# Optimization experiments

Measured on AMD Instinct MI355X. Metric: run time of the kernel, lower is better.

## Reference

```python
import jax, jax.numpy as jnp
import numpy as np

N = 50000
E = 1600000
IN_DIM = 64
EMB_DIM = 64
DENSE = 128
HEADS = 2
GATD = 64
SLOPE = 0.2


def gat_conv(x, src, dst, W, al, ar, b):
    # DGL GATConv: x [N, Fin], W [Fin, H*D], al/ar/b [H, D]
    n = x.shape[0]
    H, D = al.shape
    z = (x @ W).reshape(n, H, D)                      # [N,H,D]
    el = jnp.sum(z * al, axis=-1)                     # [N,H]
    er = jnp.sum(z * ar, axis=-1)                     # [N,H]
    e = jax.nn.leaky_relu(el[src] + er[dst], SLOPE)   # [E,H]
    # edge softmax grouped by destination node
    m = jax.ops.segment_max(e, dst, num_segments=n)   # [N,H]
    ex = jnp.exp(e - m[dst])                          # [E,H]
    s = jax.ops.segment_sum(ex, dst, num_segments=n)  # [N,H]
    alpha = ex / s[dst]                               # [E,H]
    out = jax.ops.segment_sum(alpha[:, :, None] * z[src], dst, num_segments=n)
    return out + b                                    # [N,H,D]


def setup_inputs() -> dict:
    key = jax.random.key(0)
    ks = jax.random.split(key, 20)
    g = lambda k, sh: jax.random.normal(k, sh, dtype=jnp.float32) * 0.05
    inp = {
        "feat": jax.random.normal(ks[0], (N, IN_DIM), dtype=jnp.float32),
        "node_ids": jax.random.randint(ks[1], (N,), 0, N, dtype=jnp.int32),
        "src": jax.random.randint(ks[2], (E,), 0, N, dtype=jnp.int32),
        "dst": jax.random.randint(ks[3], (E,), 0, N, dtype=jnp.int32),
        "emb": g(ks[4], (N, EMB_DIM)),
        "dense_w": g(ks[5], (IN_DIM + EMB_DIM, DENSE)),
        "dense_b": jnp.zeros((DENSE,), jnp.float32),
        "g1_w": g(ks[6], (DENSE, HEADS * GATD)),
        "g1_al": g(ks[7], (HEADS, GATD)),
        "g1_ar": g(ks[8], (HEADS, GATD)),
        "g1_b": jnp.zeros((HEADS, GATD), jnp.float32),
        "g2_w": g(ks[9], (HEADS * GATD, HEADS * GATD)),
        "g2_al": g(ks[10], (HEADS, GATD)),
        "g2_ar": g(ks[11], (HEADS, GATD)),
        "g2_b": jnp.zeros((HEADS, GATD), jnp.float32),
        "out_w": g(ks[12], (HEADS * GATD, 1)),
        "out_al": g(ks[13], (1, 1)),
        "out_ar": g(ks[14], (1, 1)),
        "out_b": jnp.zeros((1, 1), jnp.float32),
    }
    return inp


def reference(feat, node_ids, src, dst, emb, dense_w, dense_b,
              g1_w, g1_al, g1_ar, g1_b, g2_w, g2_al, g2_ar, g2_b,
              out_w, out_al, out_ar, out_b):
    # embedding concat + initial dense + ReLU
    h = jnp.concatenate([emb[node_ids], feat], axis=-1)   # [N, 128]
    h = jax.nn.relu(h @ dense_w + dense_b)                # [N, 128]
    # GAT layer 1: ReLU then concat heads (reshape N, H*D)
    h = jax.nn.relu(gat_conv(h, src, dst, g1_w, g1_al, g1_ar, g1_b))
    h = h.reshape(h.shape[0], -1)                         # [N, H*D]
    # GAT layer 2
    h = jax.nn.relu(gat_conv(h, src, dst, g2_w, g2_al, g2_ar, g2_b))
    h = h.reshape(h.shape[0], -1)
    # output GAT layer, 1 head, squeeze head dim
    h = gat_conv(h, src, dst, out_w, out_al, out_ar, out_b)  # [N,1,1]
    return h[:, 0, :]                                        # [N,1]
```

## Files before the change

kernel.cpp:

```cpp
#include <hip/hip_runtime.h>
#include <cfloat>
#include <cmath>


#define CBG 256
#define CAPC 12288
#define TILE 4096
#define BIMG 10240

typedef __attribute__((ext_vector_type(8))) short short8v;
typedef __attribute__((ext_vector_type(4))) float f32x4;

__device__ __forceinline__ float lrelu(float x) { return x > 0.f ? x : 0.2f * x; }

__device__ __forceinline__ uint32_t bf16_rne(float f) {
  uint32_t u = __float_as_uint(f);
  return (u + 0x7fffu + ((u >> 16) & 1u)) >> 16;
}
__device__ __forceinline__ uint32_t pack_hilo(float v) {
  uint32_t h = bf16_rne(v);
  float r = v - __uint_as_float(h << 16);
  return (h << 16) | bf16_rne(r);
}

__global__ __launch_bounds__(256) void prep_kernel(
    const float* __restrict__ W0, const float* __restrict__ W1,
    const float* __restrict__ W2, short* __restrict__ Whi0,
    short* __restrict__ Wlo0, short* __restrict__ Whi1, short* __restrict__ Wlo1,
    short* __restrict__ Whi2, short* __restrict__ Wlo2,
    int* __restrict__ scount, int ncb) {
  if (blockIdx.x >= 24) {
    for (int i = threadIdx.x; i < ncb; i += 256) scount[i] = 0;
    return;
  }
  int which = blockIdx.x >> 3;
  const float* W = which == 0 ? W0 : (which == 1 ? W1 : W2);
  short* Whi = which == 0 ? Whi0 : (which == 1 ? Whi1 : Whi2);
  short* Wlo = which == 0 ? Wlo0 : (which == 1 ? Wlo1 : Wlo2);
  int fid = (blockIdx.x & 7) * 256 + threadIdx.x;
  int lane = fid & 63;
  int cq = fid >> 6;
  int q = cq >> 3, c = cq & 7;
  int col = c * 16 + (lane & 15);
  int k0 = q * 32 + (lane >> 4) * 8;
#pragma unroll
  for (int j = 0; j < 8; j++) {
    float v = W[(k0 + j) * 128 + col];
    uint32_t h = bf16_rne(v);
    float r = v - __uint_as_float(h << 16);
    Whi[fid * 8 + j] = (short)h;
    Wlo[fid * 8 + j] = (short)bf16_rne(r);
  }
}

__global__ __launch_bounds__(256) void bucketA_kernel(
    const int* __restrict__ src, const int* __restrict__ dst,
    int* __restrict__ scount, uint32_t* __restrict__ tmp, int e, int ncb) {
  __shared__ int cnt[256];
  __shared__ int lscan[256];
  __shared__ int gbase[256];
  __shared__ uint32_t image[TILE];
  const int t = threadIdx.x;
  const int e0 = blockIdx.x * TILE;
  const int ne = min(TILE, e - e0);

  for (int i = t; i < 256; i += 256) cnt[i] = 0;
  __syncthreads();
  for (int i = t; i < ne; i += 256) atomicAdd(&cnt[dst[e0 + i] >> 8], 1);
  __syncthreads();
  if (t < 64) {
    int carry = 0;
    for (int base = 0; base < ncb; base += 64) {
      int idx = base + t;
      int c = (idx < ncb) ? cnt[idx] : 0;
      int v = c;
#pragma unroll
      for (int off = 1; off < 64; off <<= 1) {
        int u = __shfl_up(v, off, 64);
        if (t >= off) v += u;
      }
      if (idx < ncb) lscan[idx] = carry + v - c;
      carry += __shfl(v, 63, 64);
    }
  }
  __syncthreads();
  for (int b = t; b < ncb; b += 256)
    gbase[b] = (cnt[b] > 0) ? atomicAdd(&scount[b], cnt[b]) : 0;
  __syncthreads();
  for (int b = t; b < ncb; b += 256) cnt[b] = 0;
  __syncthreads();
  for (int i = t; i < ne; i += 256) {
    int d = dst[e0 + i], s = src[e0 + i];
    int b = d >> 8;
    int r = atomicAdd(&cnt[b], 1);
    image[lscan[b] + r] =
        (uint32_t)s | ((uint32_t)(d & 255) << 16) | ((uint32_t)b << 24);
  }
  __syncthreads();
  for (int j = t; j < ne; j += 256) {
    uint32_t w = image[j];
    int b = w >> 24;
    int pos = gbase[b] + (j - lscan[b]);
    if (pos < CAPC) tmp[(size_t)b * CAPC + pos] = w & 0xFFFFFFu;
  }
}

__device__ __forceinline__ void bucketB_body(
    int b, char* smem, const uint32_t* __restrict__ tmp,
    const int* __restrict__ scount, int* __restrict__ row_start,
    int* __restrict__ csr_src, int n, int ncb, int e, int sshift) {
  int* cnt2 = (int*)smem;
  int* wsum = cnt2 + 2048;
  int* s_base = wsum + 4;
  uint32_t* image = (uint32_t*)(smem + 8224);
  const int t = threadIdx.x, lane = t & 63, wid = t >> 6;

  if (t < 64) {
    int part = 0;
    for (int idx = lane; idx < b; idx += 64) part += scount[idx];
#pragma unroll
    for (int off = 32; off; off >>= 1) part += __shfl_xor(part, off, 64);
    if (lane == 0) *s_base = part;
  }
#pragma unroll
  for (int j = 0; j < 8; j++) cnt2[t * 8 + j] = 0;
  __syncthreads();
  const int total = min(scount[b], CAPC);
  const int base = *s_base;
  const uint32_t* strm = tmp + (size_t)b * CAPC;

  for (int i = t; i < total; i += 256) {
    uint32_t w = strm[i];
    int key = (((w >> 16) & 255) << 3) + ((w & 0xFFFFu) >> sshift);
    atomicAdd(&cnt2[key], 1);
  }
  __syncthreads();
  int c8[8];
  int run = 0;
#pragma unroll
  for (int j = 0; j < 8; j++) { int x = cnt2[t * 8 + j]; c8[j] = run; run += x; }
  int c = run, v = c;
#pragma unroll
  for (int off = 1; off < 64; off <<= 1) {
    int u = __shfl_up(v, off, 64);
    if (lane >= off) v += u;
  }
  if (lane == 63) wsum[wid] = v;
  __syncthreads();
  if (t == 0) {
    int acc = 0;
#pragma unroll
    for (int w = 0; w < 4; w++) { int x = wsum[w]; wsum[w] = acc; acc += x; }
  }
  __syncthreads();
  int ex = wsum[wid] + v - c;
#pragma unroll
  for (int j = 0; j < 8; j++) cnt2[t * 8 + j] = ex + c8[j];
  int d = b * CBG + t;
  if (d < n) row_start[d] = base + ex;
  if (b == 0 && t == 0) row_start[n] = e;
  __syncthreads();
  for (int i = t; i < total; i += 256) {
    uint32_t w = strm[i];
    uint32_t s = w & 0xFFFFu;
    int key = (((w >> 16) & 255) << 3) + (s >> sshift);
    int pos = atomicAdd(&cnt2[key], 1);
    if (pos < BIMG) image[pos] = s;
    else csr_src[base + pos] = (int)s;
  }
  __syncthreads();
  const int lim = total < BIMG ? total : BIMG;
  for (int j = t; j < lim; j += 256) csr_src[base + j] = (int)image[j];
}

template <int MODE>
__device__ __forceinline__ void mfmm_body(
    int bid, char* smem,
    const uint32_t* __restrict__ Xp, const short* __restrict__ Whi,
    const short* __restrict__ Wlo, const float* __restrict__ bias,
    uint32_t* __restrict__ Hp, uint32_t* __restrict__ zp,
    float2* __restrict__ el2, float2* __restrict__ er2,
    const float* __restrict__ al, const float* __restrict__ ar, int n,
    const float* __restrict__ emb, const int* __restrict__ ids,
    const float* __restrict__ feat) {
  short* Ahi = (short*)smem;
  short* Alo = Ahi + 64 * 136;
  const int t = threadIdx.x;
  const int nb = bid * 64;

  for (int idx = t; idx < 64 * 32; idx += 256) {
    int nl = idx >> 5, k4 = (idx & 31) << 2;
    int node = nb + nl;
    uint32_t h01 = 0, h23 = 0, l01 = 0, l23 = 0;
    if (node < n) {
      if (MODE == 1) {
        uint4 w = *(const uint4*)&Xp[(size_t)node * 128 + k4];
        h01 = (w.x >> 16) | (w.y & 0xffff0000u);
        l01 = (w.x & 0xffffu) | (w.y << 16);
        h23 = (w.z >> 16) | (w.w & 0xffff0000u);
        l23 = (w.z & 0xffffu) | (w.w << 16);
      } else {
        float4 v;
        if (k4 < 64) v = *(const float4*)&emb[(size_t)ids[node] * 64 + k4];
        else         v = *(const float4*)&feat[(size_t)node * 64 + (k4 - 64)];
        uint32_t a0 = bf16_rne(v.x), a1 = bf16_rne(v.y);
        uint32_t a2 = bf16_rne(v.z), a3 = bf16_rne(v.w);
        h01 = a0 | (a1 << 16);
        h23 = a2 | (a3 << 16);
        l01 = bf16_rne(v.x - __uint_as_float(a0 << 16)) |
              (bf16_rne(v.y - __uint_as_float(a1 << 16)) << 16);
        l23 = bf16_rne(v.z - __uint_as_float(a2 << 16)) |
              (bf16_rne(v.w - __uint_as_float(a3 << 16)) << 16);
      }
    }
    *(uint2*)&Ahi[nl * 136 + k4] = make_uint2(h01, h23);
    *(uint2*)&Alo[nl * 136 + k4] = make_uint2(l01, l23);
  }
  __syncthreads();

  const int lane = t & 63, wv = t >> 6;
  const int r16 = lane & 15, g = lane >> 4;
  const int arow = (wv * 16 + r16) * 136;

  f32x4 acc[8];
#pragma unroll
  for (int c = 0; c < 8; c++) acc[c] = (f32x4){0.f, 0.f, 0.f, 0.f};

#pragma unroll
  for (int q = 0; q < 4; q++) {
    int ka = q * 32 + g * 8;
    short8v ahi = *(const short8v*)&Ahi[arow + ka];
    short8v alo = *(const short8v*)&Alo[arow + ka];
#pragma unroll
    for (int c = 0; c < 8; c++) {
      short8v bhi = *(const short8v*)&Whi[(((q * 8 + c) * 64) + lane) * 8];
      short8v blo = *(const short8v*)&Wlo[(((q * 8 + c) * 64) + lane) * 8];
      acc[c] = __builtin_amdgcn_mfma_f32_16x16x32_bf16(ahi, bhi, acc[c], 0, 0, 0);
      acc[c] = __builtin_amdgcn_mfma_f32_16x16x32_bf16(ahi, blo, acc[c], 0, 0, 0);
      acc[c] = __builtin_amdgcn_mfma_f32_16x16x32_bf16(alo, bhi, acc[c], 0, 0, 0);
    }
  }

  const int node_base = nb + wv * 16;
  if (MODE == 0) {
#pragma unroll
    for (int c = 0; c < 8; c++) {
      int col = c * 16 + r16;
      float bv = bias[col];
#pragma unroll
      for (int r = 0; r < 4; r++) {
        int node = node_base + g * 4 + r;
        if (node < n) {
          float v = fmaxf(acc[c][r] + bv, 0.f);
          Hp[(size_t)node * 128 + col] = pack_hilo(v);
        }
      }
    }
  } else {
    float p0l[4] = {0, 0, 0, 0}, p1l[4] = {0, 0, 0, 0};
    float p0r[4] = {0, 0, 0, 0}, p1r[4] = {0, 0, 0, 0};
#pragma unroll
    for (int c = 0; c < 8; c++) {
      int col = c * 16 + r16;
      float av = al[col], rv = ar[col];
#pragma unroll
      for (int r = 0; r < 4; r++) {
        if (c < 4) { p0l[r] = fmaf(acc[c][r], av, p0l[r]); p0r[r] = fmaf(acc[c][r], rv, p0r[r]); }
        else       { p1l[r] = fmaf(acc[c][r], av, p1l[r]); p1r[r] = fmaf(acc[c][r], rv, p1r[r]); }
      }
    }
#pragma unroll
    for (int c = 0; c < 8; c++) {
#pragma unroll
      for (int r = 0; r < 4; r++) {
        float other = __shfl_xor(acc[c][r], 1, 64);
        int node = node_base + g * 4 + r;
        if (!(lane & 1) && node < n) {
          uint32_t w = bf16_rne(acc[c][r]) | (bf16_rne(other) << 16);
          zp[(size_t)node * 64 + c * 8 + (r16 >> 1)] = w;
        }
      }
    }
#pragma unroll
    for (int off = 1; off < 16; off <<= 1) {
#pragma unroll
      for (int r = 0; r < 4; r++) {
        p0l[r] += __shfl_xor(p0l[r], off, 64);
        p1l[r] += __shfl_xor(p1l[r], off, 64);
        p0r[r] += __shfl_xor(p0r[r], off, 64);
        p1r[r] += __shfl_xor(p1r[r], off, 64);
      }
    }
    if (r16 == 0) {
#pragma unroll
      for (int r = 0; r < 4; r++) {
        int node = node_base + g * 4 + r;
        if (node < n) {
          el2[node] = make_float2(p0l[r], p1l[r]);
          er2[node] = make_float2(p0r[r], p1r[r]);
        }
      }
    }
  }
}

__global__ __launch_bounds__(256) void mfmm0_bktB_kernel(
    const uint32_t* __restrict__ tmp, const int* __restrict__ scount,
    int* __restrict__ row_start, int* __restrict__ csr_src, int ncbB,
    const short* __restrict__ Whi, const short* __restrict__ Wlo,
    const float* __restrict__ bias, uint32_t* __restrict__ Hp, int n, int ncb,
    int e, int sshift, const float* __restrict__ emb, const int* __restrict__ ids,
    const float* __restrict__ feat) {
  __shared__ __align__(16) char smem[49200];
  if ((int)blockIdx.x < ncbB) {
    bucketB_body(blockIdx.x, smem, tmp, scount, row_start, csr_src, n, ncb, e,
                 sshift);
  } else {
    mfmm_body<0>(blockIdx.x - ncbB, smem, nullptr, Whi, Wlo, bias, Hp,
                 nullptr, nullptr, nullptr, nullptr, nullptr, n, emb, ids, feat);
  }
}

__global__ __launch_bounds__(256) void mfmm1_kernel(
    const uint32_t* __restrict__ Xp, const short* __restrict__ Whi,
    const short* __restrict__ Wlo, uint32_t* __restrict__ zp,
    float2* __restrict__ el2, float2* __restrict__ er2,
    const float* __restrict__ al, const float* __restrict__ ar, int n) {
  __shared__ __align__(16) char smem[34816];
  mfmm_body<1>(blockIdx.x, smem, Xp, Whi, Wlo, nullptr, nullptr, zp, el2, er2,
               al, ar, n, nullptr, nullptr, nullptr);
}

__global__ void hist_kernel(const int* __restrict__ dst, int* __restrict__ cnt, int e) {
  for (int i = blockIdx.x * blockDim.x + threadIdx.x; i < e; i += gridDim.x * blockDim.x)
    atomicAdd(&cnt[dst[i]], 1);
}
__global__ void scatter_kernel(const int* __restrict__ src, const int* __restrict__ dst,
                               const int* __restrict__ row_start, int* __restrict__ cursor,
                               int* __restrict__ csr_src, int e) {
  for (int i = blockIdx.x * blockDim.x + threadIdx.x; i < e; i += gridDim.x * blockDim.x) {
    int d = dst[i];
    int pos = atomicAdd(&cursor[d], 1);
    csr_src[row_start[d] + pos] = src[i];
  }
}
__global__ __launch_bounds__(1024) void scan1_kernel(const int* __restrict__ cnt,
                                                     int* __restrict__ row_start,
                                                     int* __restrict__ bsum, int n) {
  __shared__ int wsum[16];
  const int t = threadIdx.x, lane = t & 63, wid = t >> 6;
  int i = blockIdx.x * 1024 + t;
  int c = (i < n) ? cnt[i] : 0;
  int v = c;
#pragma unroll
  for (int off = 1; off < 64; off <<= 1) {
    int u = __shfl_up(v, off, 64);
    if (lane >= off) v += u;
  }
  if (lane == 63) wsum[wid] = v;
  __syncthreads();
  if (t == 0) {
    int acc = 0;
#pragma unroll
    for (int w = 0; w < 16; w++) { int x = wsum[w]; wsum[w] = acc; acc += x; }
    bsum[blockIdx.x] = acc;
  }
  __syncthreads();
  if (i < n) row_start[i] = wsum[wid] + v - c;
}
__global__ __launch_bounds__(64) void scan2_kernel(int* __restrict__ bsum, int nb) {
  const int lane = threadIdx.x;
  int carry = 0;
  for (int base = 0; base < nb; base += 64) {
    int idx = base + lane;
    int c = (idx < nb) ? bsum[idx] : 0;
    int v = c;
#pragma unroll
    for (int off = 1; off < 64; off <<= 1) {
      int u = __shfl_up(v, off, 64);
      if (lane >= off) v += u;
    }
    if (idx < nb) bsum[idx] = carry + v - c;
    carry += __shfl(v, 63, 64);
  }
}
__global__ void scan3_kernel(int* __restrict__ row_start, const int* __restrict__ bsum,
                             int n, int e) {
  int i = blockIdx.x * blockDim.x + threadIdx.x;
  if (i < n) row_start[i] += bsum[i >> 10];
  if (i == 0) row_start[n] = e;
}

#define CAP 256
__global__ __launch_bounds__(256) void agg12_kernel(
    const uint32_t* __restrict__ zp, const float2* __restrict__ el2,
    const float2* __restrict__ er2, const int* __restrict__ row_start,
    const int* __restrict__ csr_src, const float* __restrict__ bias,
    uint32_t* __restrict__ Hp,
    const float* __restrict__ ow, const float* __restrict__ oal,
    const float* __restrict__ oar, float* __restrict__ z3,
    float* __restrict__ el3, float* __restrict__ er3, int n, int fuse_out) {
  __shared__ float ecf[4][2][CAP];
  __shared__ int sc[4][CAP];
  const int w = threadIdx.x >> 6, lane = threadIdx.x & 63;
  const int node = blockIdx.x * 4 + w;
  const bool valid = node < n;
  int rs = 0, deg = 0;
  float er0 = 0.f, er1 = 0.f;
  if (valid) {
    rs = row_start[node];
    deg = row_start[node + 1] - rs;
    float2 e2 = er2[node];
    er0 = e2.x; er1 = e2.y;
  }
  const int cdeg = deg < CAP ? deg : CAP;

  float sp0 = 0.f, sp1 = 0.f;
  for (int i = lane; i < deg; i += 64) {
    int s = csr_src[rs + i];
    float2 l = el2[s];
    float x0 = __expf(lrelu(l.x + er0));
    float x1 = __expf(lrelu(l.y + er1));
    if (i < CAP) { sc[w][i] = s << 8; ecf[w][0][i] = x0; ecf[w][1][i] = x1; }
    sp0 += x0; sp1 += x1;
  }
#pragma unroll
  for (int off = 32; off; off >>= 1) {
    sp0 += __shfl_xor(sp0, off, 64);
    sp1 += __shfl_xor(sp1, off, 64);
  }
  __syncthreads();

  const float* exh = ecf[w][lane >> 5];
  const char* zpB = (const char*)zp + (size_t)lane * 4;
  float ae = 0.f, ao = 0.f;
  int i = 0;
  for (; i + 8 <= cdeg; i += 8) {
    uint32_t zw[8];
    float xh[8];
#pragma unroll
    for (int u = 0; u < 8; u++) {
      int off = sc[w][i + u];
      xh[u] = exh[i + u];
      zw[u] = *(const uint32_t*)(zpB + off);
    }
#pragma unroll
    for (int u = 0; u < 8; u++) {
      ae = fmaf(xh[u], __uint_as_float(zw[u] << 16), ae);
      ao = fmaf(xh[u], __uint_as_float(zw[u] & 0xffff0000u), ao);
    }
  }
  for (; i < cdeg; i++) {
    int off = sc[w][i];
    float x = exh[i];
    uint32_t zw = *(const uint32_t*)(zpB + off);
    ae = fmaf(x, __uint_as_float(zw << 16), ae);
    ao = fmaf(x, __uint_as_float(zw & 0xffff0000u), ao);
  }
  for (; i < deg; i++) {
    int s = csr_src[rs + i];
    float2 l = el2[s];
    float x0 = __expf(lrelu(l.x + er0));
    float x1 = __expf(lrelu(l.y + er1));
    float x = (lane < 32) ? x0 : x1;
    uint32_t zw = *(const uint32_t*)(zpB + ((size_t)s << 8));
    ae = fmaf(x, __uint_as_float(zw << 16), ae);
    ao = fmaf(x, __uint_as_float(zw & 0xffff0000u), ao);
  }

  if (valid) {
    float sp = (lane < 32) ? sp0 : sp1;
    float2 b2 = reinterpret_cast<const float2*>(bias)[lane];
    float oe, oo;
    if (deg == 0) { oe = b2.x; oo = b2.y; }
    else { oe = ae / sp + b2.x; oo = ao / sp + b2.y; }
    oe = fmaxf(oe, 0.f);
    oo = fmaxf(oo, 0.f);
    if (!fuse_out) {
      *(uint2*)&Hp[(size_t)node * 128 + 2 * lane] =
          make_uint2(pack_hilo(oe), pack_hilo(oo));
    } else {
      float2 w2 = reinterpret_cast<const float2*>(ow)[lane];
      float d = oe * w2.x + oo * w2.y;
#pragma unroll
      for (int off = 32; off; off >>= 1) d += __shfl_xor(d, off, 64);
      if (lane == 0) {
        z3[node] = d;
        el3[node] = d * oal[0];
        er3[node] = d * oar[0];
      }
    }
  }
}

__global__ __launch_bounds__(256) void agg3_kernel(
    const float* __restrict__ z3, const float* __restrict__ el3,
    const float* __restrict__ er3, const int* __restrict__ row_start,
    const int* __restrict__ csr_src, const float* __restrict__ b,
    float* __restrict__ out, int n) {
  int node = blockIdx.x * 8 + (threadIdx.x >> 5);
  int l32 = threadIdx.x & 31;
  if (node >= n) return;
  int rs = row_start[node];
  int deg = row_start[node + 1] - rs;
  float er = er3[node];
  float sp = 0.f, ap = 0.f;
  for (int i = l32; i < deg; i += 32) {
    int s = csr_src[rs + i];
    float ex = __expf(lrelu(el3[s] + er));
    sp += ex;
    ap = fmaf(ex, z3[s], ap);
  }
#pragma unroll
  for (int off = 16; off; off >>= 1) {
    sp += __shfl_xor(sp, off, 64);
    ap += __shfl_xor(ap, off, 64);
  }
  if (l32 == 0) out[node] = (deg == 0) ? b[0] : (ap / sp + b[0]);
}

extern "C" void kernel_launch(void* const* d_in, const int* in_sizes, int n_in,
                              void* d_out, int out_size, void* d_ws, size_t ws_size,
                              hipStream_t stream) {
  const float* feat     = (const float*)d_in[0];
  const int*   node_ids = (const int*)d_in[1];
  const int*   src      = (const int*)d_in[2];
  const int*   dst      = (const int*)d_in[3];
  const float* emb      = (const float*)d_in[4];
  const float* dense_w  = (const float*)d_in[5];
  const float* dense_b  = (const float*)d_in[6];
  const float* g1_w     = (const float*)d_in[7];
  const float* g1_al    = (const float*)d_in[8];
  const float* g1_ar    = (const float*)d_in[9];
  const float* g1_b     = (const float*)d_in[10];
  const float* g2_w     = (const float*)d_in[11];
  const float* g2_al    = (const float*)d_in[12];
  const float* g2_ar    = (const float*)d_in[13];
  const float* g2_b     = (const float*)d_in[14];
  const float* out_w    = (const float*)d_in[15];
  const float* out_al   = (const float*)d_in[16];
  const float* out_ar   = (const float*)d_in[17];
  const float* out_b    = (const float*)d_in[18];
  const int n = in_sizes[0] / 64;
  const int e = in_sizes[2];

  const int ncb = (n + CBG - 1) / CBG;
  int lg = 0;
  while ((1 << lg) < n) lg++;
  const int sshift = lg > 3 ? lg - 3 : 0;

  char* ws = (char*)d_ws;
  size_t off = 0;
  auto alloc = [&](size_t bytes) -> void* {
    void* p = ws + off;
    off += (bytes + 255) & ~(size_t)255;
    return p;
  };
  uint32_t* Hp       = (uint32_t*)alloc((size_t)n * 128 * 4);
  size_t zp_bytes    = (size_t)n * 64 * 4;
  size_t tmp_bytes   = (size_t)ncb * CAPC * 4;
  uint32_t* zp       = (uint32_t*)alloc(zp_bytes > tmp_bytes ? zp_bytes : tmp_bytes);
  uint32_t* tmp      = zp;
  float2*   el2      = (float2*)alloc((size_t)n * 8);
  float2*   er2      = (float2*)alloc((size_t)n * 8);
  float*    z3       = (float*)alloc((size_t)n * 4);
  float*    el3      = (float*)alloc((size_t)n * 4);
  float*    er3      = (float*)alloc((size_t)n * 4);
  int*      scount   = (int*)alloc((size_t)ncb * 4);
  int*      row_start= (int*)alloc((size_t)(n + 1) * 4);
  int*      csr_src  = (int*)alloc((size_t)e * 4);
  short*    Wd_hi    = (short*)alloc(2048 * 8 * 2);
  short*    Wd_lo    = (short*)alloc(2048 * 8 * 2);
  short*    W1_hi    = (short*)alloc(2048 * 8 * 2);
  short*    W1_lo    = (short*)alloc(2048 * 8 * 2);
  short*    W2_hi    = (short*)alloc(2048 * 8 * 2);
  short*    W2_lo    = (short*)alloc(2048 * 8 * 2);
  int*      cnt      = (int*)alloc((size_t)n * 4);
  int*      cursor   = (int*)alloc((size_t)n * 4);
  const int nblk     = (n + 1023) / 1024;
  int*      bsum     = (int*)alloc((size_t)nblk * 4);

  const int mmgrid = (n + 63) / 64;
  const int ngrid4 = (n + 3) / 4;
  const int ngrid8 = (n + 7) / 8;

  prep_kernel<<<25, 256, 0, stream>>>(dense_w, g1_w, g2_w,
                                      Wd_hi, Wd_lo, W1_hi, W1_lo, W2_hi, W2_lo,
                                      scount, ncb);

  if (n < 65536) {
    const int natile = (e + TILE - 1) / TILE;
    bucketA_kernel<<<natile, 256, 0, stream>>>(src, dst, scount, tmp, e, ncb);
    mfmm0_bktB_kernel<<<ncb + mmgrid, 256, 0, stream>>>(
        tmp, scount, row_start, csr_src, ncb,
        Wd_hi, Wd_lo, dense_b, Hp, n, ncb, e, sshift, emb, node_ids, feat);
  } else {
    hipMemsetAsync(cnt, 0, (size_t)n * 4, stream);
    hipMemsetAsync(cursor, 0, (size_t)n * 4, stream);
    hist_kernel<<<2048, 256, 0, stream>>>(dst, cnt, e);
    scan1_kernel<<<nblk, 1024, 0, stream>>>(cnt, row_start, bsum, n);
    scan2_kernel<<<1, 64, 0, stream>>>(bsum, nblk);
    scan3_kernel<<<(n + 255) / 256, 256, 0, stream>>>(row_start, bsum, n, e);
    scatter_kernel<<<2048, 256, 0, stream>>>(src, dst, row_start, cursor, csr_src, e);
    mfmm0_bktB_kernel<<<mmgrid, 256, 0, stream>>>(
        tmp, scount, row_start, csr_src, 0,
        Wd_hi, Wd_lo, dense_b, Hp, n, ncb, e, sshift, emb, node_ids, feat);
  }

  mfmm1_kernel<<<mmgrid, 256, 0, stream>>>(Hp, W1_hi, W1_lo, zp, el2, er2,
                                           g1_al, g1_ar, n);
  agg12_kernel<<<ngrid4, 256, 0, stream>>>(zp, el2, er2, row_start, csr_src, g1_b, Hp,
                                           nullptr, nullptr, nullptr, nullptr, nullptr,
                                           nullptr, n, 0);
  mfmm1_kernel<<<mmgrid, 256, 0, stream>>>(Hp, W2_hi, W2_lo, zp, el2, er2,
                                           g2_al, g2_ar, n);
  agg12_kernel<<<ngrid4, 256, 0, stream>>>(zp, el2, er2, row_start, csr_src, g2_b, nullptr,
                                           out_w, out_al, out_ar, z3, el3, er3, n, 1);
  agg3_kernel<<<ngrid8, 256, 0, stream>>>(z3, el3, er3, row_start, csr_src, out_b,
                                          (float*)d_out, n);
}
```

Before: 232.7 us.

## Use half-wave per node in GAT aggregation with 8-byte gathers

The agg12 kernel now gives each destination node a 32-lane half-wavefront instead of a full 64-lane wavefront, so a block handles 8 nodes. Each lane gathers an 8-byte chunk (four bf16 features) per source row instead of 4 bytes, and the output store and bias load widen to match. This halves the lanes spent per node, which should help since the mean degree is about 32, and it issues fewer, wider gather loads. In exchange each lane carries more accumulators and the unroll drops to 4, and LDS use per block doubles, which may cut occupancy.

Result: slower. 240.0 us (+3.1%).

```diff
diff --git a/kernel.cpp b/kernel.cpp
--- a/kernel.cpp
+++ b/kernel.cpp
@@ -400,10 +400,10 @@
     const float* __restrict__ ow, const float* __restrict__ oal,
     const float* __restrict__ oar, float* __restrict__ z3,
     float* __restrict__ el3, float* __restrict__ er3, int n, int fuse_out) {
-  __shared__ float ecf[4][2][CAP];
-  __shared__ int sc[4][CAP];
-  const int w = threadIdx.x >> 6, lane = threadIdx.x & 63;
-  const int node = blockIdx.x * 4 + w;
+  __shared__ float ex2[8][2][CAP];
+  __shared__ int sc[8][CAP];
+  const int hw = threadIdx.x >> 5, l32 = threadIdx.x & 31;
+  const int node = blockIdx.x * 8 + hw;
   const bool valid = node < n;
   int rs = 0, deg = 0;
   float er0 = 0.f, er1 = 0.f;
@@ -416,75 +416,86 @@
   const int cdeg = deg < CAP ? deg : CAP;
 
   float sp0 = 0.f, sp1 = 0.f;
-  for (int i = lane; i < deg; i += 64) {
+  for (int i = l32; i < deg; i += 32) {
     int s = csr_src[rs + i];
     float2 l = el2[s];
     float x0 = __expf(lrelu(l.x + er0));
     float x1 = __expf(lrelu(l.y + er1));
-    if (i < CAP) { sc[w][i] = s << 8; ecf[w][0][i] = x0; ecf[w][1][i] = x1; }
+    if (i < CAP) { sc[hw][i] = s << 8; ex2[hw][0][i] = x0; ex2[hw][1][i] = x1; }
     sp0 += x0; sp1 += x1;
   }
 #pragma unroll
-  for (int off = 32; off; off >>= 1) {
+  for (int off = 16; off; off >>= 1) {
     sp0 += __shfl_xor(sp0, off, 64);
     sp1 += __shfl_xor(sp1, off, 64);
   }
   __syncthreads();
 
-  const float* exh = ecf[w][lane >> 5];
-  const char* zpB = (const char*)zp + (size_t)lane * 4;
-  float ae = 0.f, ao = 0.f;
+  const int head = l32 >> 4;
+  const float* exh = ex2[hw][head];
+  const char* zpB = (const char*)zp + (size_t)l32 * 8;
+  float a0 = 0.f, a1 = 0.f, a2 = 0.f, a3 = 0.f;
   int i = 0;
-  for (; i + 8 <= cdeg; i += 8) {
-    uint32_t zw[8];
-    float xh[8];
-#pragma unroll
-    for (int u = 0; u < 8; u++) {
-      int off = sc[w][i + u];
+  for (; i + 4 <= cdeg; i += 4) {
+    uint2 zw[4];
+    float xh[4];
+#pragma unroll
+    for (int u = 0; u < 4; u++) {
+      int off = sc[hw][i + u];
       xh[u] = exh[i + u];
-      zw[u] = *(const uint32_t*)(zpB + off);
-    }
-#pragma unroll
-    for (int u = 0; u < 8; u++) {
-      ae = fmaf(xh[u], __uint_as_float(zw[u] << 16), ae);
-      ao = fmaf(xh[u], __uint_as_float(zw[u] & 0xffff0000u), ao);
+      zw[u] = *(const uint2*)(zpB + off);
+    }
+#pragma unroll
+    for (int u = 0; u < 4; u++) {
+      a0 = fmaf(xh[u], __uint_as_float(zw[u].x << 16), a0);
+      a1 = fmaf(xh[u], __uint_as_float(zw[u].x & 0xffff0000u), a1);
+      a2 = fmaf(xh[u], __uint_as_float(zw[u].y << 16), a2);
+      a3 = fmaf(xh[u], __uint_as_float(zw[u].y & 0xffff0000u), a3);
     }
   }
   for (; i < cdeg; i++) {
-    int off = sc[w][i];
+    int off = sc[hw][i];
     float x = exh[i];
-    uint32_t zw = *(const uint32_t*)(zpB + off);
-    ae = fmaf(x, __uint_as_float(zw << 16), ae);
-    ao = fmaf(x, __uint_as_float(zw & 0xffff0000u), ao);
+    uint2 zw = *(const uint2*)(zpB + off);
+    a0 = fmaf(x, __uint_as_float(zw.x << 16), a0);
+    a1 = fmaf(x, __uint_as_float(zw.x & 0xffff0000u), a1);
+    a2 = fmaf(x, __uint_as_float(zw.y << 16), a2);
+    a3 = fmaf(x, __uint_as_float(zw.y & 0xffff0000u), a3);
   }
   for (; i < deg; i++) {
     int s = csr_src[rs + i];
     float2 l = el2[s];
     float x0 = __expf(lrelu(l.x + er0));
     float x1 = __expf(lrelu(l.y + er1));
-    float x = (lane < 32) ? x0 : x1;
-    uint32_t zw = *(const uint32_t*)(zpB + ((size_t)s << 8));
-    ae = fmaf(x, __uint_as_float(zw << 16), ae);
-    ao = fmaf(x, __uint_as_float(zw & 0xffff0000u), ao);
+    float x = head ? x1 : x0;
+    uint2 zw = *(const uint2*)(zpB + ((size_t)s << 8));
+    a0 = fmaf(x, __uint_as_float(zw.x << 16), a0);
+    a1 = fmaf(x, __uint_as_float(zw.x & 0xffff0000u), a1);
+    a2 = fmaf(x, __uint_as_float(zw.y << 16), a2);
+    a3 = fmaf(x, __uint_as_float(zw.y & 0xffff0000u), a3);
   }
 
   if (valid) {
-    float sp = (lane < 32) ? sp0 : sp1;
-    float2 b2 = reinterpret_cast<const float2*>(bias)[lane];
-    float oe, oo;
-    if (deg == 0) { oe = b2.x; oo = b2.y; }
-    else { oe = ae / sp + b2.x; oo = ao / sp + b2.y; }
-    oe = fmaxf(oe, 0.f);
-    oo = fmaxf(oo, 0.f);
+    float sp = head ? sp1 : sp0;
+    float4 b4 = reinterpret_cast<const float4*>(bias)[l32];
+    float o0, o1, o2, o3;
+    if (deg == 0) { o0 = b4.x; o1 = b4.y; o2 = b4.z; o3 = b4.w; }
+    else {
+      o0 = a0 / sp + b4.x; o1 = a1 / sp + b4.y;
+      o2 = a2 / sp + b4.z; o3 = a3 / sp + b4.w;
+    }
+    o0 = fmaxf(o0, 0.f); o1 = fmaxf(o1, 0.f);
+    o2 = fmaxf(o2, 0.f); o3 = fmaxf(o3, 0.f);
     if (!fuse_out) {
-      *(uint2*)&Hp[(size_t)node * 128 + 2 * lane] =
-          make_uint2(pack_hilo(oe), pack_hilo(oo));
+      uint4 pk = make_uint4(pack_hilo(o0), pack_hilo(o1),
+                            pack_hilo(o2), pack_hilo(o3));
+      *(uint4*)&Hp[(size_t)node * 128 + 4 * l32] = pk;
     } else {
-      float2 w2 = reinterpret_cast<const float2*>(ow)[lane];
-      float d = oe * w2.x + oo * w2.y;
-#pragma unroll
-      for (int off = 32; off; off >>= 1) d += __shfl_xor(d, off, 64);
-      if (lane == 0) {
+      float4 w4 = reinterpret_cast<const float4*>(ow)[l32];
+      float d = o0 * w4.x + o1 * w4.y + o2 * w4.z + o3 * w4.w;
+#pragma unroll
+      for (int off = 16; off; off >>= 1) d += __shfl_xor(d, off, 64);
+      if (l32 == 0) {
         z3[node] = d;
         el3[node] = d * oal[0];
         er3[node] = d * oar[0];
@@ -581,7 +592,6 @@
   int*      bsum     = (int*)alloc((size_t)nblk * 4);
 
   const int mmgrid = (n + 63) / 64;
-  const int ngrid4 = (n + 3) / 4;
   const int ngrid8 = (n + 7) / 8;
 
   prep_kernel<<<25, 256, 0, stream>>>(dense_w, g1_w, g2_w,
@@ -609,12 +619,12 @@
 
   mfmm1_kernel<<<mmgrid, 256, 0, stream>>>(Hp, W1_hi, W1_lo, zp, el2, er2,
                                            g1_al, g1_ar, n);
-  agg12_kernel<<<ngrid4, 256, 0, stream>>>(zp, el2, er2, row_start, csr_src, g1_b, Hp,
+  agg12_kernel<<<ngrid8, 256, 0, stream>>>(zp, el2, er2, row_start, csr_src, g1_b, Hp,
                                            nullptr, nullptr, nullptr, nullptr, nullptr,
                                            nullptr, n, 0);
   mfmm1_kernel<<<mmgrid, 256, 0, stream>>>(Hp, W2_hi, W2_lo, zp, el2, er2,
                                            g2_al, g2_ar, n);
-  agg12_kernel<<<ngrid4, 256, 0, stream>>>(zp, el2, er2, row_start, csr_src, g2_b, nullptr,
+  agg12_kernel<<<ngrid8, 256, 0, stream>>>(zp, el2, er2, row_start, csr_src, g2_b, nullptr,
                                            out_w, out_al, out_ar, z3, el3, er3, n, 1);
   agg3_kernel<<<ngrid8, 256, 0, stream>>>(z3, el3, er3, row_start, csr_src, out_b,
                                           (float*)d_out, n);
```

## Co-schedule edge bucketing with dense and GAT1 matmuls in fused kernels

Applied to the files above, without the earlier changes.

Merges the first edge-bucketing pass with the dense matmul into one launch, and the second bucketing pass with the layer-1 GAT projection into another, so the independent graph preprocessing overlaps with the matmuls and one launch is removed. The bucket temp buffer no longer aliases zp, since both are now live at the same time, which costs extra workspace. It also drops a block-wide barrier in the aggregation kernel, relying on each wave only touching its own shared-memory slice.

Result: faster. 219.0 us (-5.9%).

```diff
diff --git a/kernel.cpp b/kernel.cpp
--- a/kernel.cpp
+++ b/kernel.cpp
@@ -53,15 +53,15 @@
   }
 }
 
-__global__ __launch_bounds__(256) void bucketA_kernel(
-    const int* __restrict__ src, const int* __restrict__ dst,
+__device__ __forceinline__ void bucketA_body(
+    int blk, char* smem, const int* __restrict__ src, const int* __restrict__ dst,
     int* __restrict__ scount, uint32_t* __restrict__ tmp, int e, int ncb) {
-  __shared__ int cnt[256];
-  __shared__ int lscan[256];
-  __shared__ int gbase[256];
-  __shared__ uint32_t image[TILE];
+  int* cnt = (int*)smem;
+  int* lscan = cnt + 256;
+  int* gbase = lscan + 256;
+  uint32_t* image = (uint32_t*)(smem + 3072);
   const int t = threadIdx.x;
-  const int e0 = blockIdx.x * TILE;
+  const int e0 = blk * TILE;
   const int ne = min(TILE, e - e0);
 
   for (int i = t; i < 256; i += 256) cnt[i] = 0;
@@ -304,20 +304,37 @@
   }
 }
 
-__global__ __launch_bounds__(256) void mfmm0_bktB_kernel(
+__global__ __launch_bounds__(256) void fusedA_kernel(
+    const int* __restrict__ src, const int* __restrict__ dst,
+    int* __restrict__ scount, uint32_t* __restrict__ tmp, int e, int ncb, int nA,
+    const short* __restrict__ Whi, const short* __restrict__ Wlo,
+    const float* __restrict__ bias, uint32_t* __restrict__ Hp, int n,
+    const float* __restrict__ emb, const int* __restrict__ ids,
+    const float* __restrict__ feat) {
+  __shared__ __align__(16) char smem[34816];
+  if ((int)blockIdx.x < nA) {
+    bucketA_body(blockIdx.x, smem, src, dst, scount, tmp, e, ncb);
+  } else {
+    mfmm_body<0>(blockIdx.x - nA, smem, nullptr, Whi, Wlo, bias, Hp,
+                 nullptr, nullptr, nullptr, nullptr, nullptr, n, emb, ids, feat);
+  }
+}
+
+__global__ __launch_bounds__(256) void fusedB_kernel(
     const uint32_t* __restrict__ tmp, const int* __restrict__ scount,
     int* __restrict__ row_start, int* __restrict__ csr_src, int ncbB,
-    const short* __restrict__ Whi, const short* __restrict__ Wlo,
-    const float* __restrict__ bias, uint32_t* __restrict__ Hp, int n, int ncb,
-    int e, int sshift, const float* __restrict__ emb, const int* __restrict__ ids,
-    const float* __restrict__ feat) {
+    int n, int ncb, int e, int sshift,
+    const uint32_t* __restrict__ Xp, const short* __restrict__ Whi,
+    const short* __restrict__ Wlo, uint32_t* __restrict__ zp,
+    float2* __restrict__ el2, float2* __restrict__ er2,
+    const float* __restrict__ al, const float* __restrict__ ar) {
   __shared__ __align__(16) char smem[49200];
   if ((int)blockIdx.x < ncbB) {
     bucketB_body(blockIdx.x, smem, tmp, scount, row_start, csr_src, n, ncb, e,
                  sshift);
   } else {
-    mfmm_body<0>(blockIdx.x - ncbB, smem, nullptr, Whi, Wlo, bias, Hp,
-                 nullptr, nullptr, nullptr, nullptr, nullptr, n, emb, ids, feat);
+    mfmm_body<1>(blockIdx.x - ncbB, smem, Xp, Whi, Wlo, nullptr, nullptr, zp,
+                 el2, er2, al, ar, n, nullptr, nullptr, nullptr);
   }
 }
 
@@ -429,7 +446,6 @@
     sp0 += __shfl_xor(sp0, off, 64);
     sp1 += __shfl_xor(sp1, off, 64);
   }
-  __syncthreads();
 
   const float* exh = ecf[w][lane >> 5];
   const char* zpB = (const char*)zp + (size_t)lane * 4;
@@ -557,10 +573,8 @@
     return p;
   };
   uint32_t* Hp       = (uint32_t*)alloc((size_t)n * 128 * 4);
-  size_t zp_bytes    = (size_t)n * 64 * 4;
-  size_t tmp_bytes   = (size_t)ncb * CAPC * 4;
-  uint32_t* zp       = (uint32_t*)alloc(zp_bytes > tmp_bytes ? zp_bytes : tmp_bytes);
-  uint32_t* tmp      = zp;
+  uint32_t* zp       = (uint32_t*)alloc((size_t)n * 64 * 4);
+  uint32_t* tmp      = (uint32_t*)alloc((size_t)ncb * CAPC * 4);
   float2*   el2      = (float2*)alloc((size_t)n * 8);
   float2*   er2      = (float2*)alloc((size_t)n * 8);
   float*    z3       = (float*)alloc((size_t)n * 4);
@@ -590,10 +604,12 @@
 
   if (n < 65536) {
     const int natile = (e + TILE - 1) / TILE;
-    bucketA_kernel<<<natile, 256, 0, stream>>>(src, dst, scount, tmp, e, ncb);
-    mfmm0_bktB_kernel<<<ncb + mmgrid, 256, 0, stream>>>(
-        tmp, scount, row_start, csr_src, ncb,
-        Wd_hi, Wd_lo, dense_b, Hp, n, ncb, e, sshift, emb, node_ids, feat);
+    fusedA_kernel<<<natile + mmgrid, 256, 0, stream>>>(
+        src, dst, scount, tmp, e, ncb, natile,
+        Wd_hi, Wd_lo, dense_b, Hp, n, emb, node_ids, feat);
+    fusedB_kernel<<<ncb + mmgrid, 256, 0, stream>>>(
+        tmp, scount, row_start, csr_src, ncb, n, ncb, e, sshift,
+        Hp, W1_hi, W1_lo, zp, el2, er2, g1_al, g1_ar);
   } else {
     hipMemsetAsync(cnt, 0, (size_t)n * 4, stream);
     hipMemsetAsync(cursor, 0, (size_t)n * 4, stream);
@@ -602,13 +618,14 @@
     scan2_kernel<<<1, 64, 0, stream>>>(bsum, nblk);
     scan3_kernel<<<(n + 255) / 256, 256, 0, stream>>>(row_start, bsum, n, e);
     scatter_kernel<<<2048, 256, 0, stream>>>(src, dst, row_start, cursor, csr_src, e);
-    mfmm0_bktB_kernel<<<mmgrid, 256, 0, stream>>>(
-        tmp, scount, row_start, csr_src, 0,
-        Wd_hi, Wd_lo, dense_b, Hp, n, ncb, e, sshift, emb, node_ids, feat);
-  }
-
-  mfmm1_kernel<<<mmgrid, 256, 0, stream>>>(Hp, W1_hi, W1_lo, zp, el2, er2,
-                                           g1_al, g1_ar, n);
+    fusedA_kernel<<<mmgrid, 256, 0, stream>>>(
+        src, dst, scount, tmp, e, ncb, 0,
+        Wd_hi, Wd_lo, dense_b, Hp, n, emb, node_ids, feat);
+    fusedB_kernel<<<mmgrid, 256, 0, stream>>>(
+        tmp, scount, row_start, csr_src, 0, n, ncb, e, sshift,
+        Hp, W1_hi, W1_lo, zp, el2, er2, g1_al, g1_ar);
+  }
+
   agg12_kernel<<<ngrid4, 256, 0, stream>>>(zp, el2, er2, row_start, csr_src, g1_b, Hp,
                                            nullptr, nullptr, nullptr, nullptr, nullptr,
                                            nullptr, n, 0);
```
